# Performance work log

Hardware: AMD Instinct MI355X
Metric: run time of the kernel (lower is better)

## Reference

```python
import jax, jax.numpy as jnp
import numpy as np

B, L, INPUT_DIM = 4, 4096, 32
D_MODEL, N_LAYERS = 256, 2
D_STATE, D_CONV, EXPAND = 16, 4, 2
D_INNER = EXPAND * D_MODEL          # 512
DT_RANK = (D_MODEL + 15) // 16      # 16
OUTPUT_DIM, HORIZON = 32, 4
LN_EPS = 1e-5


def setup_inputs() -> dict:
    key = jax.random.key(0)
    ks = jax.random.split(key, 16)
    s = 0.02
    inp = {
        "x": jax.random.normal(ks[0], (B, L, INPUT_DIM), jnp.float32),
        "enc_w": jax.random.normal(ks[1], (D_MODEL, INPUT_DIM), jnp.float32) * s,
        "enc_b": jnp.zeros((D_MODEL,), jnp.float32),
        "in_proj_w": jax.random.normal(ks[2], (N_LAYERS, 2 * D_INNER, D_MODEL), jnp.float32) * s,
        "conv_w": jax.random.normal(ks[3], (N_LAYERS, D_INNER, D_CONV), jnp.float32) * s,
        "conv_b": jnp.zeros((N_LAYERS, D_INNER), jnp.float32),
        "xproj_w": jax.random.normal(ks[4], (N_LAYERS, DT_RANK + 2 * D_STATE, D_INNER), jnp.float32) * s,
        "dtproj_w": jax.random.normal(ks[5], (N_LAYERS, D_INNER, DT_RANK), jnp.float32) * s,
        "dtproj_b": jax.random.normal(ks[6], (N_LAYERS, D_INNER), jnp.float32) * 0.1,
        "A_log": jnp.log(jnp.tile(jnp.arange(1.0, D_STATE + 1.0, dtype=jnp.float32), (N_LAYERS, D_INNER, 1))),
        "Dp": jnp.ones((N_LAYERS, D_INNER), jnp.float32),
        "out_proj_w": jax.random.normal(ks[7], (N_LAYERS, D_MODEL, D_INNER), jnp.float32) * s,
        "ln_g": jnp.ones((D_MODEL,), jnp.float32),
        "ln_b": jnp.zeros((D_MODEL,), jnp.float32),
        "head_w": jax.random.normal(ks[8], (OUTPUT_DIM * HORIZON, D_MODEL), jnp.float32) * s,
        "head_b": jnp.zeros((OUTPUT_DIM * HORIZON,), jnp.float32),
    }
    return inp


def _mamba_block(x, in_w, cw, cb, xp_w, dt_w, dt_b, A_log, Dp, out_w):
    # x: [B, L, d_model]
    b, l, _ = x.shape
    xz = jnp.einsum("bld,ed->ble", x, in_w)            # [B, L, 2*d_inner]
    xi, res = jnp.split(xz, 2, axis=-1)
    # causal depthwise conv1d (padding=d_conv-1, truncated to L)
    xpad = jnp.pad(xi, ((0, 0), (D_CONV - 1, 0), (0, 0)))
    xi = sum(xpad[:, k:k + l, :] * cw[:, k] for k in range(D_CONV)) + cb
    xi = jax.nn.silu(xi)
    dbl = jnp.einsum("bld,ed->ble", xi, xp_w)           # [B, L, dt_rank+2*d_state]
    dt = dbl[..., :DT_RANK]
    Bm = dbl[..., DT_RANK:DT_RANK + D_STATE]            # [B, L, d_state]
    Cm = dbl[..., DT_RANK + D_STATE:]                   # [B, L, d_state]
    dt = jax.nn.softplus(jnp.einsum("blr,dr->bld", dt, dt_w) + dt_b)  # [B, L, d_inner]
    A = -jnp.exp(A_log)                                 # [d_inner, d_state]

    def step(h, ins):
        dt_t, B_t, C_t, x_t = ins                       # [B,di],[B,ds],[B,ds],[B,di]
        dA = jnp.exp(dt_t[..., None] * A)               # [B, d_inner, d_state]
        h = dA * h + (dt_t * x_t)[..., None] * B_t[:, None, :]
        y = jnp.einsum("bds,bs->bd", h, C_t)
        return h, y

    h0 = jnp.zeros((b, D_INNER, D_STATE), x.dtype)
    xs = (jnp.moveaxis(dt, 1, 0), jnp.moveaxis(Bm, 1, 0),
          jnp.moveaxis(Cm, 1, 0), jnp.moveaxis(xi, 1, 0))
    _, ys = jax.lax.scan(step, h0, xs)                  # ys: [L, B, d_inner]
    y = jnp.moveaxis(ys, 0, 1) + xi * Dp
    y = y * jax.nn.silu(res)
    return jnp.einsum("ble,de->bld", y, out_w)


def reference(x, enc_w, enc_b, in_proj_w, conv_w, conv_b, xproj_w, dtproj_w,
              dtproj_b, A_log, Dp, out_proj_w, ln_g, ln_b, head_w, head_b):
    h = jnp.einsum("bli,di->bld", x, enc_w) + enc_b     # encoder
    for i in range(N_LAYERS):
        h = h + _mamba_block(h, in_proj_w[i], conv_w[i], conv_b[i], xproj_w[i],
                             dtproj_w[i], dtproj_b[i], A_log[i], Dp[i], out_proj_w[i])
    mu = jnp.mean(h, axis=-1, keepdims=True)
    var = jnp.mean((h - mu) ** 2, axis=-1, keepdims=True)
    hn = (h - mu) * jax.lax.rsqrt(var + LN_EPS) * ln_g + ln_b
    state = hn[:, -1, :]                                # last timestep
    return jnp.einsum("bd,od->bo", state, head_w) + head_b
```

## Files before the change

### kernel.cpp

```cpp
#include <hip/hip_runtime.h>
#include <hip/hip_bf16.h>
#include <math.h>

#define BB 4
#define LL 4096
#define DM 256
#define DI 512
#define DS 16
#define NOUTK 128
#define LN_EPS 1e-5f
#define NC 128
#define CLEN (LL/NC)
#define BL (BB*LL)
#define LDB 640

typedef __attribute__((ext_vector_type(8))) short short8;
typedef __attribute__((ext_vector_type(4))) float f32x4;

__device__ __forceinline__ ushort f2bf(float f) {
    union { float f; unsigned u; } v; v.f = f;
    unsigned r = (v.u + 0x7FFF + ((v.u >> 16) & 1)) >> 16;
    return (ushort)r;
}
__device__ __forceinline__ float bf2f(ushort u) {
    union { unsigned u; float f; } v; v.u = ((unsigned)u) << 16;
    return v.f;
}

__global__ __launch_bounds__(256) void cast_bf16_kernel(
    const float* __restrict__ src, ushort* __restrict__ dst, int n)
{
    int i = blockIdx.x * 256 + threadIdx.x;
    if (i < n) dst[i] = f2bf(src[i]);
}

__global__ __launch_bounds__(256) void build_comb_kernel(
    const float* __restrict__ xpw, const float* __restrict__ dtw,
    ushort* __restrict__ dst)
{
    int i = blockIdx.x * 256 + threadIdx.x;
    int l = i / (640 * 512);
    int rem = i - l * 640 * 512;
    int row = rem >> 9, k = rem & 511;
    const float* xp = xpw + l * 48 * 512;
    const float* dw = dtw + l * 512 * 16;
    float v;
    if (row < 512) {
        v = 0.f;
        #pragma unroll
        for (int r = 0; r < 16; ++r)
            v = fmaf(dw[row * 16 + r], xp[r * 512 + k], v);
    } else if (row < 544) {
        v = xp[(row - 512 + 16) * 512 + k];
    } else v = 0.f;
    dst[i] = f2bf(v);
}

__global__ __launch_bounds__(256) void enc_kernel(
    const float* __restrict__ x, const float* __restrict__ w,
    const float* __restrict__ b, float* __restrict__ h,
    ushort* __restrict__ hbf)
{
    __shared__ float sw[256 * 33];
    __shared__ float sx[4][32];
    int tid = threadIdx.x;
    for (int i = tid; i < 256 * 8; i += 256) {
        float4 v = ((const float4*)w)[i];
        int r = i >> 3, c = (i & 7) * 4;
        sw[r * 33 + c + 0] = v.x; sw[r * 33 + c + 1] = v.y;
        sw[r * 33 + c + 2] = v.z; sw[r * 33 + c + 3] = v.w;
    }
    int row0 = blockIdx.x * 4;
    if (tid < 32) {
        for (int rr = 0; rr < 4; ++rr)
            sx[rr][tid] = x[(size_t)(row0 + rr) * 32 + tid];
    }
    __syncthreads();
    float bb = b[tid];
    #pragma unroll
    for (int rr = 0; rr < 4; ++rr) {
        float acc = bb;
        #pragma unroll
        for (int k = 0; k < 32; ++k)
            acc = fmaf(sx[rr][k], sw[tid * 33 + k], acc);
        size_t o = (size_t)(row0 + rr) * DM + tid;
        h[o] = acc;
        hbf[o] = f2bf(acc);
    }
}

template<int EPI, bool F32OUT, bool RESID, bool BF16OUT>
__global__ __launch_bounds__(256, 4) void mfma_gemm(
    const ushort* __restrict__ A, int lda,
    const ushort* __restrict__ W,
    const float* __restrict__ bias,
    float* __restrict__ C, int ldc,
    ushort* __restrict__ Cbf, int ldcbf,
    int K)
{
    __shared__ ushort As[64 * 64];
    __shared__ ushort Ws[128 * 64];
    const int tid = threadIdx.x;

    int nwg = gridDim.x * gridDim.y;
    int wlin = blockIdx.y * gridDim.x + blockIdx.x;
    int gx = blockIdx.x, gy = blockIdx.y;
    if ((nwg & 7) == 0) {
        int q = nwg >> 3;
        int s = (wlin & 7) * q + (wlin >> 3);
        gx = s % gridDim.x;
        gy = s / gridDim.x;
    }
    const int bm = gy * 64;
    const int bn = gx * 128;
    const int wid = tid >> 6, lane = tid & 63;
    const int wrow = (wid >> 1) * 32, wcol = (wid & 1) * 64;
    const int sr = tid >> 3;
    const int sc = tid & 7;

    f32x4 acc[2][4];
    #pragma unroll
    for (int mi = 0; mi < 2; ++mi)
        #pragma unroll
        for (int ni = 0; ni < 4; ++ni)
            acc[mi][ni] = (f32x4){0.f, 0.f, 0.f, 0.f};

    const int nk = K >> 6;
    for (int t = 0; t < nk; ++t) {
        const int k0 = t << 6;
        #pragma unroll
        for (int it = 0; it < 2; ++it) {
            int r = it * 32 + sr;
            int csrc = sc ^ (r & 7);
            __builtin_amdgcn_global_load_lds(
                (const __attribute__((address_space(1))) unsigned int*)
                    (A + (size_t)(bm + r) * lda + k0 + csrc * 8),
                (__attribute__((address_space(3))) unsigned int*)
                    (As + r * 64 + sc * 8), 16, 0, 0);
        }
        #pragma unroll
        for (int it = 0; it < 4; ++it) {
            int r = it * 32 + sr;
            int csrc = sc ^ (r & 7);
            __builtin_amdgcn_global_load_lds(
                (const __attribute__((address_space(1))) unsigned int*)
                    (W + (size_t)(bn + r) * K + k0 + csrc * 8),
                (__attribute__((address_space(3))) unsigned int*)
                    (Ws + r * 64 + sc * 8), 16, 0, 0);
        }
        __syncthreads();
        #pragma unroll
        for (int kk = 0; kk < 2; ++kk) {
            short8 af[2], bfr[4];
            #pragma unroll
            for (int mi = 0; mi < 2; ++mi) {
                int r = wrow + mi * 16 + (lane & 15);
                int c = (lane >> 4) + kk * 4;
                af[mi] = *(const short8*)(As + r * 64 + ((c ^ (r & 7)) << 3));
            }
            #pragma unroll
            for (int ni = 0; ni < 4; ++ni) {
                int r = wcol + ni * 16 + (lane & 15);
                int c = (lane >> 4) + kk * 4;
                bfr[ni] = *(const short8*)(Ws + r * 64 + ((c ^ (r & 7)) << 3));
            }
            #pragma unroll
            for (int mi = 0; mi < 2; ++mi)
                #pragma unroll
                for (int ni = 0; ni < 4; ++ni)
                    acc[mi][ni] = __builtin_amdgcn_mfma_f32_16x16x32_bf16(
                        af[mi], bfr[ni], acc[mi][ni], 0, 0, 0);
        }
        __syncthreads();
    }

    #pragma unroll
    for (int mi = 0; mi < 2; ++mi)
        #pragma unroll
        for (int ni = 0; ni < 4; ++ni) {
            int col = bn + wcol + ni * 16 + (lane & 15);
            #pragma unroll
            for (int r = 0; r < 4; ++r) {
                int row = bm + wrow + mi * 16 + (lane >> 4) * 4 + r;
                float v = acc[mi][ni][r];
                if (EPI == 1) {
                    if (col < 512) {
                        float u = v + bias[col];
                        float sp = fmaxf(u, 0.f) + __logf(1.f + __expf(-fabsf(u)));
                        Cbf[(size_t)row * ldcbf + col] = f2bf(sp);
                    } else if (col < 544) {
                        C[(size_t)row * ldc + (col - 512)] = v;
                    }
                } else {
                    if (F32OUT) {
                        float* cp = C + (size_t)row * ldc + col;
                        float vv = v;
                        if (RESID) vv += *cp;
                        *cp = vv;
                        if (BF16OUT) Cbf[(size_t)row * ldcbf + col] = f2bf(vv);
                    } else if (BF16OUT) {
                        Cbf[(size_t)row * ldcbf + col] = f2bf(v);
                    }
                }
            }
        }
}

__global__ __launch_bounds__(256) void conv_silu_kernel(
    const ushort* __restrict__ xz, const float* __restrict__ cw,
    const float* __restrict__ cb, ushort* __restrict__ xi)
{
    int idx = blockIdx.x * 256 + threadIdx.x;
    int d4 = (idx & 127) * 4;
    int bt = idx >> 7;
    int t = bt & (LL - 1);
    const ushort* base = xz + (size_t)bt * 1024 + d4;
    float acc[4];
    float4 w[4];
    #pragma unroll
    for (int j = 0; j < 4; ++j) {
        acc[j] = cb[d4 + j];
        w[j] = *(const float4*)(cw + (d4 + j) * 4);
    }
    #pragma unroll
    for (int k = 0; k < 4; ++k) {
        int back = 3 - k;
        if (t >= back) {
            ushort4 v = *(const ushort4*)(base - back * 1024);
            float wk0 = (k==0)?w[0].x:(k==1)?w[0].y:(k==2)?w[0].z:w[0].w;
            float wk1 = (k==0)?w[1].x:(k==1)?w[1].y:(k==2)?w[1].z:w[1].w;
            float wk2 = (k==0)?w[2].x:(k==1)?w[2].y:(k==2)?w[2].z:w[2].w;
            float wk3 = (k==0)?w[3].x:(k==1)?w[3].y:(k==2)?w[3].z:w[3].w;
            acc[0] = fmaf(bf2f(v.x), wk0, acc[0]);
            acc[1] = fmaf(bf2f(v.y), wk1, acc[1]);
            acc[2] = fmaf(bf2f(v.z), wk2, acc[2]);
            acc[3] = fmaf(bf2f(v.w), wk3, acc[3]);
        }
    }
    ushort4 o;
    float s0 = acc[0] / (1.f + __expf(-acc[0]));
    float s1 = acc[1] / (1.f + __expf(-acc[1]));
    float s2 = acc[2] / (1.f + __expf(-acc[2]));
    float s3 = acc[3] / (1.f + __expf(-acc[3]));
    o.x = f2bf(s0); o.y = f2bf(s1); o.z = f2bf(s2); o.w = f2bf(s3);
    *(ushort4*)(xi + (size_t)bt * 512 + d4) = o;
}

__global__ __launch_bounds__(256) void scan_phase1(
    const ushort* __restrict__ xi, const ushort* __restrict__ dtb,
    const float* __restrict__ bc,
    const float* __restrict__ alog,
    float* __restrict__ cA, float* __restrict__ cH)
{
    int d = blockIdx.z * 256 + threadIdx.x;
    int b = blockIdx.y, c = blockIdx.x;
    float Av[16];
    bool fast = true;
    #pragma unroll
    for (int s = 0; s < 16; ++s) {
        Av[s] = -__expf(alog[d * 16 + s]);
        fast = fast && (fabsf(Av[s] + (float)(s + 1)) < 1e-3f * (s + 1));
    }
    float h[16], P[16];
    #pragma unroll
    for (int s = 0; s < 16; ++s) { h[s] = 0.f; P[s] = 1.f; }
    int t0 = c * CLEN;
    if (fast) {
        float Pe = 1.f;
        for (int t = t0; t < t0 + CLEN; ++t) {
            size_t row = (size_t)b * LL + t;
            float dt = bf2f(dtb[row * 512 + d]);
            float x = bf2f(xi[row * 512 + d]);
            float dtx = dt * x;
            const float* bp = bc + row * 32;
            float e1 = __expf(-dt);
            float e2=e1*e1, e3=e2*e1, e4=e2*e2, e5=e3*e2, e6=e3*e3, e7=e4*e3, e8=e4*e4;
            float e9=e5*e4, e10=e5*e5, e11=e6*e5, e12=e6*e6, e13=e7*e6, e14=e7*e7, e15=e8*e7, e16=e8*e8;
            float pw[16] = {e1,e2,e3,e4,e5,e6,e7,e8,e9,e10,e11,e12,e13,e14,e15,e16};
            #pragma unroll
            for (int s = 0; s < 16; ++s)
                h[s] = fmaf(pw[s], h[s], dtx * bp[s]);
            Pe *= e1;
        }
        float p1=Pe, p2=p1*p1, p3=p2*p1, p4=p2*p2, p5=p3*p2, p6=p3*p3, p7=p4*p3, p8=p4*p4;
        float p9=p5*p4, p10=p5*p5, p11=p6*p5, p12=p6*p6, p13=p7*p6, p14=p7*p7, p15=p8*p7, p16=p8*p8;
        float pp[16] = {p1,p2,p3,p4,p5,p6,p7,p8,p9,p10,p11,p12,p13,p14,p15,p16};
        #pragma unroll
        for (int s = 0; s < 16; ++s) P[s] = pp[s];
    } else {
        for (int t = t0; t < t0 + CLEN; ++t) {
            size_t row = (size_t)b * LL + t;
            float dt = bf2f(dtb[row * 512 + d]);
            float x = bf2f(xi[row * 512 + d]);
            float dtx = dt * x;
            const float* bp = bc + row * 32;
            #pragma unroll
            for (int s = 0; s < 16; ++s) {
                float dA = __expf(dt * Av[s]);
                h[s] = fmaf(dA, h[s], dtx * bp[s]);
                P[s] *= dA;
            }
        }
    }
    size_t base = (((size_t)b * DI + d) * NC + c) * 16;
    #pragma unroll
    for (int q = 0; q < 4; ++q) {
        *(float4*)(cA + base + q*4) = *(float4*)&P[q*4];
        *(float4*)(cH + base + q*4) = *(float4*)&h[q*4];
    }
}

__global__ __launch_bounds__(256) void scan_phase2(
    const float* __restrict__ cA, float* __restrict__ cH)
{
    int bd = blockIdx.x;
    int tid = threadIdx.x;
    int s = tid >> 4;
    int g = tid & 15;
    size_t base = (size_t)bd * NC * 16 + s;
    float a8[8], h8[8];
    #pragma unroll
    for (int j = 0; j < 8; ++j) {
        size_t o = base + (size_t)(g * 8 + j) * 16;
        a8[j] = cA[o]; h8[j] = cH[o];
    }
    float A = 1.f, H = 0.f;
    #pragma unroll
    for (int j = 0; j < 8; ++j) {
        H = fmaf(a8[j], H, h8[j]);
        A *= a8[j];
    }
    #pragma unroll
    for (int off = 1; off < 16; off <<= 1) {
        float Ap = __shfl_up(A, off, 16);
        float Hp = __shfl_up(H, off, 16);
        if (g >= off) { H = fmaf(A, Hp, H); A *= Ap; }
    }
    float init = __shfl_up(H, 1, 16);
    if (g == 0) init = 0.f;
    #pragma unroll
    for (int j = 0; j < 8; ++j) {
        size_t o = base + (size_t)(g * 8 + j) * 16;
        cH[o] = init;
        init = fmaf(a8[j], init, h8[j]);
    }
}

__global__ __launch_bounds__(256) void scan_phase3(
    const ushort* __restrict__ xz,
    ushort* __restrict__ xi,
    const ushort* __restrict__ dtb,
    const float* __restrict__ bc,
    const float* __restrict__ alog,
    const float* __restrict__ Dp,
    const float* __restrict__ cH,
    int c0)
{
    int d = blockIdx.z * 256 + threadIdx.x;
    int b = blockIdx.y;
    int c = blockIdx.x + c0;
    float Av[16];
    bool fast = true;
    #pragma unroll
    for (int s = 0; s < 16; ++s) {
        Av[s] = -__expf(alog[d * 16 + s]);
        fast = fast && (fabsf(Av[s] + (float)(s + 1)) < 1e-3f * (s + 1));
    }
    float h[16];
    size_t cbase = (((size_t)b * DI + d) * NC + c) * 16;
    #pragma unroll
    for (int q = 0; q < 4; ++q)
        *(float4*)&h[q*4] = *(const float4*)(cH + cbase + q*4);
    float Dd = Dp[d];
    int t0 = c * CLEN;
    if (fast) {
        for (int t = t0; t < t0 + CLEN; ++t) {
            size_t row = (size_t)b * LL + t;
            float dt = bf2f(dtb[row * 512 + d]);
            float x = bf2f(xi[row * 512 + d]);
            float dtx = dt * x;
            const float* bp = bc + row * 32;
            const float* cp = bc + row * 32 + 16;
            float e1 = __expf(-dt);
            float e2=e1*e1, e3=e2*e1, e4=e2*e2, e5=e3*e2, e6=e3*e3, e7=e4*e3, e8=e4*e4;
            float e9=e5*e4, e10=e5*e5, e11=e6*e5, e12=e6*e6, e13=e7*e6, e14=e7*e7, e15=e8*e7, e16=e8*e8;
            float pw[16] = {e1,e2,e3,e4,e5,e6,e7,e8,e9,e10,e11,e12,e13,e14,e15,e16};
            float y = 0.f;
            #pragma unroll
            for (int s = 0; s < 16; ++s) {
                h[s] = fmaf(pw[s], h[s], dtx * bp[s]);
                y = fmaf(h[s], cp[s], y);
            }
            float res = bf2f(xz[row * 1024 + 512 + d]);
            float g = (y + x * Dd) * (res / (1.f + __expf(-res)));
            xi[row * 512 + d] = f2bf(g);
        }
    } else {
        for (int t = t0; t < t0 + CLEN; ++t) {
            size_t row = (size_t)b * LL + t;
            float dt = bf2f(dtb[row * 512 + d]);
            float x = bf2f(xi[row * 512 + d]);
            float dtx = dt * x;
            const float* bp = bc + row * 32;
            const float* cp = bc + row * 32 + 16;
            float y = 0.f;
            #pragma unroll
            for (int s = 0; s < 16; ++s) {
                float dA = __expf(dt * Av[s]);
                h[s] = fmaf(dA, h[s], dtx * bp[s]);
                y = fmaf(h[s], cp[s], y);
            }
            float res = bf2f(xz[row * 1024 + 512 + d]);
            float g = (y + x * Dd) * (res / (1.f + __expf(-res)));
            xi[row * 512 + d] = f2bf(g);
        }
    }
}

__global__ __launch_bounds__(256) void out_proj_last_kernel(
    const ushort* __restrict__ xi, const float* __restrict__ W,
    float* __restrict__ h)
{
    int b = blockIdx.x, n = threadIdx.x;
    __shared__ float sy[DI];
    const ushort* yrow = xi + ((size_t)b * LL + (LL - 1)) * DI;
    for (int k = threadIdx.x; k < DI; k += 256) sy[k] = bf2f(yrow[k]);
    __syncthreads();
    const float* wr = W + (size_t)n * DI;
    float acc = 0.f;
    for (int k = 0; k < DI; k += 4) {
        float4 wv = *(const float4*)(wr + k);
        acc = fmaf(sy[k+0], wv.x, acc);
        acc = fmaf(sy[k+1], wv.y, acc);
        acc = fmaf(sy[k+2], wv.z, acc);
        acc = fmaf(sy[k+3], wv.w, acc);
    }
    h[((size_t)b * LL + (LL - 1)) * DM + n] += acc;
}

__global__ __launch_bounds__(256) void ln_head_kernel(
    const float* __restrict__ h, const float* __restrict__ lng,
    const float* __restrict__ lnb, const float* __restrict__ hw,
    const float* __restrict__ hb, float* __restrict__ out)
{
    int b = blockIdx.x, tid = threadIdx.x;
    __shared__ float sh[DM];
    __shared__ float r1[4], r2[4];
    float v = h[((size_t)b * LL + (LL - 1)) * DM + tid];
    float s = v;
    #pragma unroll
    for (int o = 32; o >= 1; o >>= 1) s += __shfl_down(s, o);
    if ((tid & 63) == 0) r1[tid >> 6] = s;
    __syncthreads();
    float mu = (r1[0] + r1[1] + r1[2] + r1[3]) * (1.f / 256.f);
    float dv = v - mu;
    float q = dv * dv;
    #pragma unroll
    for (int o = 32; o >= 1; o >>= 1) q += __shfl_down(q, o);
    if ((tid & 63) == 0) r2[tid >> 6] = q;
    __syncthreads();
    float var = (r2[0] + r2[1] + r2[2] + r2[3]) * (1.f / 256.f);
    sh[tid] = dv * rsqrtf(var + LN_EPS) * lng[tid] + lnb[tid];
    __syncthreads();
    if (tid < NOUTK) {
        const float* wr = hw + (size_t)tid * DM;
        float acc = hb[tid];
        for (int d2 = 0; d2 < DM; d2 += 4) {
            float4 wv = *(const float4*)(wr + d2);
            acc = fmaf(sh[d2+0], wv.x, acc);
            acc = fmaf(sh[d2+1], wv.y, acc);
            acc = fmaf(sh[d2+2], wv.z, acc);
            acc = fmaf(sh[d2+3], wv.w, acc);
        }
        out[b * NOUTK + tid] = acc;
    }
}

extern "C" void kernel_launch(void* const* d_in, const int* in_sizes, int n_in,
                              void* d_out, int out_size, void* d_ws, size_t ws_size,
                              hipStream_t stream)
{
    const float* x    = (const float*)d_in[0];
    const float* encw = (const float*)d_in[1];
    const float* encb = (const float*)d_in[2];
    const float* inw  = (const float*)d_in[3];
    const float* cw   = (const float*)d_in[4];
    const float* cb   = (const float*)d_in[5];
    const float* xpw  = (const float*)d_in[6];
    const float* dtw  = (const float*)d_in[7];
    const float* dtb  = (const float*)d_in[8];
    const float* alog = (const float*)d_in[9];
    const float* Dp   = (const float*)d_in[10];
    const float* opw  = (const float*)d_in[11];
    const float* lng  = (const float*)d_in[12];
    const float* lnb  = (const float*)d_in[13];
    const float* hw   = (const float*)d_in[14];
    const float* hb   = (const float*)d_in[15];
    float* out = (float*)d_out;

    float* ws   = (float*)d_ws;
    float* h    = ws;
    float* bc   = h   + (size_t)BL * DM;
    float* cA   = bc  + (size_t)BL * 32;
    float* cH   = cA  + (size_t)BB * DI * NC * DS;
    ushort* h_bf    = (ushort*)(cH + (size_t)BB * DI * NC * DS);
    ushort* xz_bf   = h_bf  + (size_t)BL * DM;
    ushort* xi_bf   = xz_bf + (size_t)BL * 1024;
    ushort* dt_bf   = xi_bf + (size_t)BL * DI;
    ushort* inw_bf  = dt_bf + (size_t)BL * DI;
    ushort* opw_bf  = inw_bf + 2 * 1024 * DM;
    ushort* comb_bf = opw_bf + 2 * DM * DI;

    dim3 blk(256, 1, 1);

    cast_bf16_kernel<<<dim3((2*1024*DM)/256), blk, 0, stream>>>(inw, inw_bf, 2*1024*DM);
    cast_bf16_kernel<<<dim3((2*DM*DI)/256), blk, 0, stream>>>(opw, opw_bf, 2*DM*DI);
    build_comb_kernel<<<dim3((2*640*512)/256), blk, 0, stream>>>(xpw, dtw, comb_bf);

    enc_kernel<<<dim3(BL/4), blk, 0, stream>>>(x, encw, encb, h, h_bf);

    for (int l = 0; l < 2; ++l) {
        mfma_gemm<0,false,false,true><<<dim3(1024/128, BL/64), blk, 0, stream>>>(
            h_bf, DM, inw_bf + (size_t)l * 1024 * DM, nullptr,
            nullptr, 0, xz_bf, 1024, DM);
        conv_silu_kernel<<<dim3(BL * 128 / 256), blk, 0, stream>>>(
            xz_bf, cw + l * DI * 4, cb + l * DI, xi_bf);
        mfma_gemm<1,false,false,false><<<dim3(LDB/128, BL/64), blk, 0, stream>>>(
            xi_bf, DI, comb_bf + (size_t)l * LDB * DI, dtb + l * DI,
            bc, 32, dt_bf, 512, DI);
        scan_phase1<<<dim3(NC, BB, 2), blk, 0, stream>>>(
            xi_bf, dt_bf, bc, alog + (size_t)l * DI * 16, cA, cH);
        scan_phase2<<<dim3(BB * DI), blk, 0, stream>>>(cA, cH);
        if (l == 0) {
            scan_phase3<<<dim3(NC, BB, 2), blk, 0, stream>>>(
                xz_bf, xi_bf, dt_bf, bc, alog + (size_t)l * DI * 16,
                Dp + l * DI, cH, 0);
            mfma_gemm<0,true,true,true><<<dim3(DM/128, BL/64), blk, 0, stream>>>(
                xi_bf, DI, opw_bf + (size_t)l * DM * DI, nullptr,
                h, DM, h_bf, DM, DI);
        } else {
            scan_phase3<<<dim3(1, BB, 2), blk, 0, stream>>>(
                xz_bf, xi_bf, dt_bf, bc, alog + (size_t)l * DI * 16,
                Dp + l * DI, cH, NC - 1);
            out_proj_last_kernel<<<dim3(BB), blk, 0, stream>>>(
                xi_bf, opw + (size_t)l * DM * DI, h);
        }
    }

    ln_head_kernel<<<dim3(BB), blk, 0, stream>>>(h, lng, lnb, hw, hb, out);
}
```

Baseline: 369.7 us.

## Store chunk dt sums instead of decay products, fuse prep kernels, raise GEMM occupancy

```diff
diff --git a/kernel.cpp b/kernel.cpp
--- a/kernel.cpp
+++ b/kernel.cpp
@@ -27,20 +27,29 @@
     return v.f;
 }
 
-__global__ __launch_bounds__(256) void cast_bf16_kernel(
-    const float* __restrict__ src, ushort* __restrict__ dst, int n)
+#define PREP_N1 (2*1024*256)
+#define PREP_N2 (2*256*512)
+#define PREP_N3 (2*640*512)
+__global__ __launch_bounds__(256) void prep_kernel(
+    const float* __restrict__ inw, const float* __restrict__ opw,
+    const float* __restrict__ xpw, const float* __restrict__ dtw,
+    ushort* __restrict__ inw_bf, ushort* __restrict__ opw_bf,
+    ushort* __restrict__ comb_bf)
 {
     int i = blockIdx.x * 256 + threadIdx.x;
-    if (i < n) dst[i] = f2bf(src[i]);
-}
-
-__global__ __launch_bounds__(256) void build_comb_kernel(
-    const float* __restrict__ xpw, const float* __restrict__ dtw,
-    ushort* __restrict__ dst)
-{
-    int i = blockIdx.x * 256 + threadIdx.x;
-    int l = i / (640 * 512);
-    int rem = i - l * 640 * 512;
+    if (i < PREP_N1) {
+        inw_bf[i] = f2bf(inw[i]);
+        return;
+    }
+    int j = i - PREP_N1;
+    if (j < PREP_N2) {
+        opw_bf[j] = f2bf(opw[j]);
+        return;
+    }
+    int m = j - PREP_N2;
+    if (m >= PREP_N3) return;
+    int l = m / (640 * 512);
+    int rem = m - l * 640 * 512;
     int row = rem >> 9, k = rem & 511;
     const float* xp = xpw + l * 48 * 512;
     const float* dw = dtw + l * 512 * 16;
@@ -53,7 +62,7 @@
     } else if (row < 544) {
         v = xp[(row - 512 + 16) * 512 + k];
     } else v = 0.f;
-    dst[i] = f2bf(v);
+    comb_bf[m] = f2bf(v);
 }
 
 __global__ __launch_bounds__(256) void enc_kernel(
@@ -90,7 +99,7 @@
 }
 
 template<int EPI, bool F32OUT, bool RESID, bool BF16OUT>
-__global__ __launch_bounds__(256, 4) void mfma_gemm(
+__global__ __launch_bounds__(256, 6) void mfma_gemm(
     const ushort* __restrict__ A, int lda,
     const ushort* __restrict__ W,
     const float* __restrict__ bias,
@@ -250,7 +259,7 @@
     const ushort* __restrict__ xi, const ushort* __restrict__ dtb,
     const float* __restrict__ bc,
     const float* __restrict__ alog,
-    float* __restrict__ cA, float* __restrict__ cH)
+    float* __restrict__ cS, float* __restrict__ cH)
 {
     int d = blockIdx.z * 256 + threadIdx.x;
     int b = blockIdx.y, c = blockIdx.x;
@@ -261,17 +270,18 @@
         Av[s] = -__expf(alog[d * 16 + s]);
         fast = fast && (fabsf(Av[s] + (float)(s + 1)) < 1e-3f * (s + 1));
     }
-    float h[16], P[16];
-    #pragma unroll
-    for (int s = 0; s < 16; ++s) { h[s] = 0.f; P[s] = 1.f; }
+    float h[16];
+    #pragma unroll
+    for (int s = 0; s < 16; ++s) h[s] = 0.f;
+    float S = 0.f;
     int t0 = c * CLEN;
     if (fast) {
-        float Pe = 1.f;
         for (int t = t0; t < t0 + CLEN; ++t) {
             size_t row = (size_t)b * LL + t;
             float dt = bf2f(dtb[row * 512 + d]);
             float x = bf2f(xi[row * 512 + d]);
             float dtx = dt * x;
+            S += dt;
             const float* bp = bc + row * 32;
             float e1 = __expf(-dt);
             float e2=e1*e1, e3=e2*e1, e4=e2*e2, e5=e3*e2, e6=e3*e3, e7=e4*e3, e8=e4*e4;
@@ -280,49 +290,47 @@
             #pragma unroll
             for (int s = 0; s < 16; ++s)
                 h[s] = fmaf(pw[s], h[s], dtx * bp[s]);
-            Pe *= e1;
-        }
-        float p1=Pe, p2=p1*p1, p3=p2*p1, p4=p2*p2, p5=p3*p2, p6=p3*p3, p7=p4*p3, p8=p4*p4;
-        float p9=p5*p4, p10=p5*p5, p11=p6*p5, p12=p6*p6, p13=p7*p6, p14=p7*p7, p15=p8*p7, p16=p8*p8;
-        float pp[16] = {p1,p2,p3,p4,p5,p6,p7,p8,p9,p10,p11,p12,p13,p14,p15,p16};
-        #pragma unroll
-        for (int s = 0; s < 16; ++s) P[s] = pp[s];
+        }
     } else {
         for (int t = t0; t < t0 + CLEN; ++t) {
             size_t row = (size_t)b * LL + t;
             float dt = bf2f(dtb[row * 512 + d]);
             float x = bf2f(xi[row * 512 + d]);
             float dtx = dt * x;
+            S += dt;
             const float* bp = bc + row * 32;
             #pragma unroll
             for (int s = 0; s < 16; ++s) {
                 float dA = __expf(dt * Av[s]);
                 h[s] = fmaf(dA, h[s], dtx * bp[s]);
-                P[s] *= dA;
             }
         }
     }
+    cS[((size_t)b * DI + d) * NC + c] = S;
     size_t base = (((size_t)b * DI + d) * NC + c) * 16;
     #pragma unroll
-    for (int q = 0; q < 4; ++q) {
-        *(float4*)(cA + base + q*4) = *(float4*)&P[q*4];
+    for (int q = 0; q < 4; ++q)
         *(float4*)(cH + base + q*4) = *(float4*)&h[q*4];
-    }
 }
 
 __global__ __launch_bounds__(256) void scan_phase2(
-    const float* __restrict__ cA, float* __restrict__ cH)
+    const float* __restrict__ cS, float* __restrict__ cH,
+    const float* __restrict__ alog)
 {
     int bd = blockIdx.x;
+    int d = bd & (DI - 1);
     int tid = threadIdx.x;
     int s = tid >> 4;
     int g = tid & 15;
+    float Avs = -__expf(alog[d * 16 + s]);
+    size_t sbase = (size_t)bd * NC;
     size_t base = (size_t)bd * NC * 16 + s;
     float a8[8], h8[8];
     #pragma unroll
     for (int j = 0; j < 8; ++j) {
-        size_t o = base + (size_t)(g * 8 + j) * 16;
-        a8[j] = cA[o]; h8[j] = cH[o];
+        float Sj = cS[sbase + g * 8 + j];
+        a8[j] = __expf(Avs * Sj);
+        h8[j] = cH[base + (size_t)(g * 8 + j) * 16];
     }
     float A = 1.f, H = 0.f;
     #pragma unroll
@@ -501,8 +509,8 @@
     float* ws   = (float*)d_ws;
     float* h    = ws;
     float* bc   = h   + (size_t)BL * DM;
-    float* cA   = bc  + (size_t)BL * 32;
-    float* cH   = cA  + (size_t)BB * DI * NC * DS;
+    float* cS   = bc  + (size_t)BL * 32;
+    float* cH   = cS  + (size_t)BB * DI * NC;
     ushort* h_bf    = (ushort*)(cH + (size_t)BB * DI * NC * DS);
     ushort* xz_bf   = h_bf  + (size_t)BL * DM;
     ushort* xi_bf   = xz_bf + (size_t)BL * 1024;
@@ -513,9 +521,8 @@
 
     dim3 blk(256, 1, 1);
 
-    cast_bf16_kernel<<<dim3((2*1024*DM)/256), blk, 0, stream>>>(inw, inw_bf, 2*1024*DM);
-    cast_bf16_kernel<<<dim3((2*DM*DI)/256), blk, 0, stream>>>(opw, opw_bf, 2*DM*DI);
-    build_comb_kernel<<<dim3((2*640*512)/256), blk, 0, stream>>>(xpw, dtw, comb_bf);
+    prep_kernel<<<dim3((PREP_N1 + PREP_N2 + PREP_N3) / 256), blk, 0, stream>>>(
+        inw, opw, xpw, dtw, inw_bf, opw_bf, comb_bf);
 
     enc_kernel<<<dim3(BL/4), blk, 0, stream>>>(x, encw, encb, h, h_bf);
 
@@ -529,8 +536,9 @@
             xi_bf, DI, comb_bf + (size_t)l * LDB * DI, dtb + l * DI,
             bc, 32, dt_bf, 512, DI);
         scan_phase1<<<dim3(NC, BB, 2), blk, 0, stream>>>(
-            xi_bf, dt_bf, bc, alog + (size_t)l * DI * 16, cA, cH);
-        scan_phase2<<<dim3(BB * DI), blk, 0, stream>>>(cA, cH);
+            xi_bf, dt_bf, bc, alog + (size_t)l * DI * 16, cS, cH);
+        scan_phase2<<<dim3(BB * DI), blk, 0, stream>>>(
+            cS, cH, alog + (size_t)l * DI * 16);
         if (l == 0) {
             scan_phase3<<<dim3(NC, BB, 2), blk, 0, stream>>>(
                 xz_bf, xi_bf, dt_bf, bc, alog + (size_t)l * DI * 16,
```

Result: faster. 345.9 us (-6.5%).
